# Kernel tuning notes

Hardware: AMD Instinct MI355X
Metric: run time of the kernel (lower is better)

Reference implementation:

```python
import jax, jax.numpy as jnp
import numpy as np

NUM_LABELS = 3   # init kwarg num_labels
# init kwarg p = 1.0 -> always equalize (deterministic reference)
NUM_BINS = 256


def _equalize_channel(chan):
    """Torchvision-style histogram equalization of one uint8 channel.

    chan: int32 [H, W] with values in [0, 255].
    """
    # per-channel histogram (scatter-add into 256 bins)
    hist = jnp.zeros(NUM_BINS, jnp.int32).at[chan.ravel()].add(1)
    total = hist.sum()
    # value at the last nonzero bin: nonzero_hist[:-1].sum() == total - hist[last_nonzero]
    last_nz = (NUM_BINS - 1) - jnp.argmax((hist > 0)[::-1])
    step = (total - hist[last_nz]) // (NUM_BINS - 1)
    # LUT = floor((cumsum(hist) + step//2) / step), shifted right by one, clamped
    cum = jnp.cumsum(hist)
    lut = (cum + step // 2) // jnp.maximum(step, 1)
    lut = jnp.clip(jnp.concatenate([jnp.zeros(1, lut.dtype), lut[:-1]]), 0, NUM_BINS - 1)
    # step == 0 -> identity (torchvision early-return)
    return jnp.where(step == 0, chan, lut[chan])


def setup_inputs() -> dict:
    key = jax.random.key(0)
    # 3 RGB-like channels in [0, 255) + 3 label channels, CHW
    image = jax.random.uniform(key, (3 + NUM_LABELS, 2048, 4096), jnp.float32) * 255.0
    return {"image": image}


def reference(image):
    sample = image[:-NUM_LABELS].astype(jnp.int32)   # mimics .to(torch.uint8) truncation
    targets = image[-NUM_LABELS:]
    sample_eq = jax.vmap(_equalize_channel)(sample).astype(jnp.float32)
    return jnp.concatenate([sample_eq, targets], axis=0)
```

## Files before the change

kernel.cpp:

```cpp
#include <hip/hip_runtime.h>

#define IMG_H 2048
#define IMG_W 4096
#define CH_ELEMS (IMG_H * IMG_W)
#define CH_N4    (CH_ELEMS / 4)
#define NUM_CH 6
#define SAMPLE_CH 3
#define HBINS 256
#define BPC 512

#define WS_LUT_OFF  (2u << 20)
#define WS_U8_OFF   (4u << 20)

__global__ __launch_bounds__(256) void eq_pass1_kernel(
        const float* __restrict__ in, float* __restrict__ out,
        unsigned* __restrict__ u8buf, int* __restrict__ parts) {
    const int t   = threadIdx.x;
    const int ch  = blockIdx.x / BPC;
    const int blk = blockIdx.x % BPC;

    if (ch >= SAMPLE_CH) {
        const float4* src = (const float4*)(in + (size_t)ch * CH_ELEMS);
        float4*       dst = (float4*)(out + (size_t)ch * CH_ELEMS);
        for (int i = blk * 256 + t; i < CH_N4; i += BPC * 256)
            dst[i] = src[i];
        return;
    }

    __shared__ int lh[4][HBINS];
    const int wave = t >> 6;
    for (int i = t; i < 4 * HBINS; i += 256) ((int*)lh)[i] = 0;
    __syncthreads();

    const float4* src = (const float4*)(in + (size_t)ch * CH_ELEMS);
    unsigned*     dst = u8buf + ch * CH_N4;

    for (int i = blk * 256 + t; i < CH_N4; i += BPC * 256) {
        float4 v = src[i];
        int b0 = (int)v.x; b0 = min(max(b0, 0), 255);
        int b1 = (int)v.y; b1 = min(max(b1, 0), 255);
        int b2 = (int)v.z; b2 = min(max(b2, 0), 255);
        int b3 = (int)v.w; b3 = min(max(b3, 0), 255);
        atomicAdd(&lh[wave][b0], 1);
        atomicAdd(&lh[wave][b1], 1);
        atomicAdd(&lh[wave][b2], 1);
        atomicAdd(&lh[wave][b3], 1);
        dst[i] = (unsigned)b0 | ((unsigned)b1 << 8) |
                 ((unsigned)b2 << 16) | ((unsigned)b3 << 24);
    }
    __syncthreads();

    parts[((size_t)ch * BPC + blk) * HBINS + t] =
        lh[0][t] + lh[1][t] + lh[2][t] + lh[3][t];
}

__global__ __launch_bounds__(256) void eq_lut_kernel(
        const int* __restrict__ parts, float* __restrict__ glut) {
    const int ch = blockIdx.x;
    const int t  = threadIdx.x;
    const int* p = parts + (size_t)ch * BPC * HBINS;

    int h = 0;
    #pragma unroll 8
    for (int j = 0; j < BPC; j++) h += p[j * HBINS + t];

    __shared__ int sh[HBINS];
    __shared__ int sc[HBINS];
    __shared__ int nz[HBINS];
    sh[t] = h;
    sc[t] = h;
    nz[t] = (h > 0) ? t : 0;
    __syncthreads();

    for (int off = 1; off < HBINS; off <<= 1) {
        int add = (t >= off) ? sc[t - off] : 0;
        __syncthreads();
        sc[t] += add;
        __syncthreads();
    }
    for (int off = HBINS / 2; off >= 1; off >>= 1) {
        if (t < off) nz[t] = max(nz[t], nz[t + off]);
        __syncthreads();
    }

    const int total   = sc[HBINS - 1];
    const int last_nz = nz[0];
    const int step    = (total - sh[last_nz]) / (HBINS - 1);

    float outv;
    if (step == 0) {
        outv = (float)t;
    } else if (t == 0) {
        outv = 0.0f;
    } else {
        int v = (sc[t - 1] + (step >> 1)) / step;
        outv = (float)min(v, 255);
    }
    glut[ch * HBINS + t] = outv;
}

__global__ __launch_bounds__(256) void eq_apply_kernel(
        const unsigned* __restrict__ u8buf, const float* __restrict__ glut,
        float* __restrict__ out) {
    __shared__ float sl[SAMPLE_CH * HBINS];
    for (int i = threadIdx.x; i < SAMPLE_CH * HBINS; i += 256)
        sl[i] = glut[i];
    __syncthreads();

    float4* out4 = (float4*)out;
    const int n = SAMPLE_CH * CH_N4;

    for (int i = blockIdx.x * 256 + threadIdx.x; i < n; i += gridDim.x * 256) {
        unsigned w = u8buf[i];
        const float* l = sl + (i >> 21) * HBINS;
        float4 o;
        o.x = l[w & 255u];
        o.y = l[(w >> 8) & 255u];
        o.z = l[(w >> 16) & 255u];
        o.w = l[w >> 24];
        out4[i] = o;
    }
}

extern "C" void kernel_launch(void* const* d_in, const int* in_sizes, int n_in,
                              void* d_out, int out_size, void* d_ws, size_t ws_size,
                              hipStream_t stream) {
    const float* image = (const float*)d_in[0];
    float* out = (float*)d_out;

    int*      parts = (int*)d_ws;
    float*    lut   = (float*)((char*)d_ws + WS_LUT_OFF);
    unsigned* u8buf = (unsigned*)((char*)d_ws + WS_U8_OFF);

    eq_pass1_kernel<<<NUM_CH * BPC, 256, 0, stream>>>(image, out, u8buf, parts);
    eq_lut_kernel<<<SAMPLE_CH, 256, 0, stream>>>(parts, lut);
    eq_apply_kernel<<<2048, 256, 0, stream>>>(u8buf, lut, out);
}
```

Measured before the change: 368.7 us.

## Fuse histogram, LUT and apply into one cooperative kernel keeping pixels in registers

Replaces the three-kernel pipeline with one cooperative kernel. Each thread loads its sample pixels once, builds per-wave shared histograms and keeps the packed bytes in registers. After grid syncs it merges into a global histogram with atomics, and every block redundantly computes the LUTs before writing output. This removes the u8 intermediate buffer round-trip and two launches. The cost is two grid-wide barriers, 24 live registers per thread that limit occupancy, and a copy of the label channels delayed until the end. Falls back to the old path if the cooperative launch fails.

```diff
diff --git a/kernel.cpp b/kernel.cpp
--- a/kernel.cpp
+++ b/kernel.cpp
@@ -1,4 +1,7 @@
 #include <hip/hip_runtime.h>
+#include <hip/hip_cooperative_groups.h>
+
+namespace cg = cooperative_groups;
 
 #define IMG_H 2048
 #define IMG_W 4096
@@ -7,10 +10,115 @@
 #define NUM_CH 6
 #define SAMPLE_CH 3
 #define HBINS 256
+
+#define GRID 1024
+#define TPB  256
+#define NTHREADS (GRID * TPB)
+#define F4PT (CH_N4 / NTHREADS)
+
 #define BPC 512
-
 #define WS_LUT_OFF  (2u << 20)
 #define WS_U8_OFF   (4u << 20)
+
+__global__ __launch_bounds__(TPB, 4) void eq_fused_kernel(
+        const float* __restrict__ in, float* __restrict__ out,
+        int* __restrict__ gh) {
+    cg::grid_group grid = cg::this_grid();
+    const int t    = threadIdx.x;
+    const int gid  = blockIdx.x * TPB + t;
+    const int wave = t >> 6;
+
+    __shared__ int   lh[4][SAMPLE_CH][HBINS];
+    __shared__ float slut[SAMPLE_CH][HBINS];
+    __shared__ int   sc[HBINS];
+    __shared__ int   sh2[HBINS];
+    __shared__ int   nzr[HBINS];
+
+    for (int i = t; i < 4 * SAMPLE_CH * HBINS; i += TPB) ((int*)lh)[i] = 0;
+    if (blockIdx.x == 0)
+        for (int i = t; i < SAMPLE_CH * HBINS; i += TPB) gh[i] = 0;
+    __syncthreads();
+
+    unsigned pk[SAMPLE_CH][F4PT];
+    const float4* in4 = (const float4*)in;
+    #pragma unroll
+    for (int ch = 0; ch < SAMPLE_CH; ch++) {
+        #pragma unroll
+        for (int j = 0; j < F4PT; j++) {
+            float4 v = in4[(size_t)ch * CH_N4 + j * NTHREADS + gid];
+            int b0 = (int)v.x; b0 = min(max(b0, 0), 255);
+            int b1 = (int)v.y; b1 = min(max(b1, 0), 255);
+            int b2 = (int)v.z; b2 = min(max(b2, 0), 255);
+            int b3 = (int)v.w; b3 = min(max(b3, 0), 255);
+            atomicAdd(&lh[wave][ch][b0], 1);
+            atomicAdd(&lh[wave][ch][b1], 1);
+            atomicAdd(&lh[wave][ch][b2], 1);
+            atomicAdd(&lh[wave][ch][b3], 1);
+            pk[ch][j] = (unsigned)b0 | ((unsigned)b1 << 8) |
+                        ((unsigned)b2 << 16) | ((unsigned)b3 << 24);
+        }
+    }
+    __syncthreads();
+
+    grid.sync();
+
+    for (int i = t; i < SAMPLE_CH * HBINS; i += TPB) {
+        int ch = i >> 8, b = i & 255;
+        int s = lh[0][ch][b] + lh[1][ch][b] + lh[2][ch][b] + lh[3][ch][b];
+        if (s) atomicAdd(&gh[i], s);
+    }
+
+    grid.sync();
+
+    for (int ch = 0; ch < SAMPLE_CH; ch++) {
+        int h = gh[ch * HBINS + t];
+        sh2[t] = h; sc[t] = h; nzr[t] = (h > 0) ? t : 0;
+        __syncthreads();
+        for (int off = 1; off < HBINS; off <<= 1) {
+            int add = (t >= off) ? sc[t - off] : 0;
+            __syncthreads();
+            sc[t] += add;
+            __syncthreads();
+        }
+        for (int off = HBINS / 2; off >= 1; off >>= 1) {
+            if (t < off) nzr[t] = max(nzr[t], nzr[t + off]);
+            __syncthreads();
+        }
+        const int total   = sc[HBINS - 1];
+        const int last_nz = nzr[0];
+        const int step    = (total - sh2[last_nz]) / (HBINS - 1);
+        float ov;
+        if (step == 0)      ov = (float)t;
+        else if (t == 0)    ov = 0.0f;
+        else                ov = (float)min((sc[t - 1] + (step >> 1)) / step, 255);
+        slut[ch][t] = ov;
+        __syncthreads();
+    }
+
+    float4* out4 = (float4*)out;
+    #pragma unroll
+    for (int ch = 0; ch < SAMPLE_CH; ch++) {
+        const float* l = slut[ch];
+        #pragma unroll
+        for (int j = 0; j < F4PT; j++) {
+            unsigned w = pk[ch][j];
+            float4 o;
+            o.x = l[w & 255u];
+            o.y = l[(w >> 8) & 255u];
+            o.z = l[(w >> 16) & 255u];
+            o.w = l[w >> 24];
+            out4[(size_t)ch * CH_N4 + j * NTHREADS + gid] = o;
+        }
+    }
+    #pragma unroll
+    for (int ch = SAMPLE_CH; ch < NUM_CH; ch++) {
+        #pragma unroll
+        for (int j = 0; j < F4PT; j++) {
+            size_t idx = (size_t)ch * CH_N4 + j * NTHREADS + gid;
+            out4[idx] = in4[idx];
+        }
+    }
+}
 
 __global__ __launch_bounds__(256) void eq_pass1_kernel(
         const float* __restrict__ in, float* __restrict__ out,
@@ -67,9 +175,7 @@
     __shared__ int sh[HBINS];
     __shared__ int sc[HBINS];
     __shared__ int nz[HBINS];
-    sh[t] = h;
-    sc[t] = h;
-    nz[t] = (h > 0) ? t : 0;
+    sh[t] = h; sc[t] = h; nz[t] = (h > 0) ? t : 0;
     __syncthreads();
 
     for (int off = 1; off < HBINS; off <<= 1) {
@@ -88,14 +194,9 @@
     const int step    = (total - sh[last_nz]) / (HBINS - 1);
 
     float outv;
-    if (step == 0) {
-        outv = (float)t;
-    } else if (t == 0) {
-        outv = 0.0f;
-    } else {
-        int v = (sc[t - 1] + (step >> 1)) / step;
-        outv = (float)min(v, 255);
-    }
+    if (step == 0)      outv = (float)t;
+    else if (t == 0)    outv = 0.0f;
+    else                outv = (float)min((sc[t - 1] + (step >> 1)) / step, 255);
     glut[ch * HBINS + t] = outv;
 }
 
@@ -127,12 +228,18 @@
                               hipStream_t stream) {
     const float* image = (const float*)d_in[0];
     float* out = (float*)d_out;
-
-    int*      parts = (int*)d_ws;
-    float*    lut   = (float*)((char*)d_ws + WS_LUT_OFF);
-    unsigned* u8buf = (unsigned*)((char*)d_ws + WS_U8_OFF);
-
-    eq_pass1_kernel<<<NUM_CH * BPC, 256, 0, stream>>>(image, out, u8buf, parts);
-    eq_lut_kernel<<<SAMPLE_CH, 256, 0, stream>>>(parts, lut);
-    eq_apply_kernel<<<2048, 256, 0, stream>>>(u8buf, lut, out);
-}
+    int* gh = (int*)d_ws;
+
+    void* args[] = { (void*)&image, (void*)&out, (void*)&gh };
+    hipError_t err = hipLaunchCooperativeKernel(
+        (const void*)eq_fused_kernel, dim3(GRID), dim3(TPB), args, 0, stream);
+
+    if (err != hipSuccess) {
+        int*      parts = (int*)((char*)d_ws + (16u << 10));
+        float*    lut   = (float*)((char*)d_ws + WS_LUT_OFF);
+        unsigned* u8buf = (unsigned*)((char*)d_ws + WS_U8_OFF);
+        eq_pass1_kernel<<<NUM_CH * BPC, 256, 0, stream>>>(image, out, u8buf, parts);
+        eq_lut_kernel<<<SAMPLE_CH, 256, 0, stream>>>(parts, lut);
+        eq_apply_kernel<<<2048, 256, 0, stream>>>(u8buf, lut, out);
+    }
+}
```

Result: slower. 552.2 us (+49.8%).
